# Kernel tuning notes

Measured on AMD Instinct MI355X. Metric: run time of the kernel, lower is better.

Reference implementation:

```python
import jax, jax.numpy as jnp
import numpy as np

DIM = 3072
HEADS = 24
HEAD_DIM = 128
INNER = HEADS * HEAD_DIM
EPS = 1e-6
B, IMG_LEN, TXT_LEN = 1, 2048, 512
S = IMG_LEN + TXT_LEN


def setup_inputs() -> dict:
    key = jax.random.key(0)
    ks = jax.random.split(key, 16)
    w = lambda k, shp: (jax.random.normal(k, shp, dtype=jnp.float32) * 0.02)
    return {
        "x": jax.random.normal(ks[0], (B, IMG_LEN, DIM), dtype=jnp.float32),
        "ctx": jax.random.normal(ks[1], (B, TXT_LEN, DIM), dtype=jnp.float32),
        "rope_cos": jax.random.uniform(ks[2], (S, HEAD_DIM), dtype=jnp.float32),
        "rope_sin": jax.random.uniform(ks[3], (S, HEAD_DIM), dtype=jnp.float32),
        "wq": w(ks[4], (INNER, DIM)),
        "wk": w(ks[5], (INNER, DIM)),
        "wv": w(ks[6], (INNER, DIM)),
        "gq": jnp.ones((HEAD_DIM,), jnp.float32),
        "gk": jnp.ones((HEAD_DIM,), jnp.float32),
        "wo": w(ks[7], (DIM, INNER)),
        "awq": w(ks[8], (INNER, DIM)),
        "awk": w(ks[9], (INNER, DIM)),
        "awv": w(ks[10], (INNER, DIM)),
        "agq": jnp.ones((HEAD_DIM,), jnp.float32),
        "agk": jnp.ones((HEAD_DIM,), jnp.float32),
        "awo": w(ks[11], (DIM, INNER)),
    }


def _rms_norm(t, g):
    # t: [b, s, h, d]; normalize over last dim
    var = jnp.mean(t * t, axis=-1, keepdims=True)
    return t * jax.lax.rsqrt(var + EPS) * g


def _heads(t):
    # [b, s, h*d] -> [b, s, h, d]
    b, s, _ = t.shape
    return t.reshape(b, s, HEADS, HEAD_DIM)


def _apply_rope(t, cos, sin):
    # t: [b, s, h, d]; cos/sin: [s, d] interleaved-pair layout (diffusers Flux style)
    b, s, h, d = t.shape
    x = t.reshape(b, s, h, d // 2, 2)
    rot = jnp.stack([-x[..., 1], x[..., 0]], axis=-1).reshape(b, s, h, d)
    c = cos[None, :, None, :]
    si = sin[None, :, None, :]
    return t * c + rot * si


def reference(x, ctx, rope_cos, rope_sin, wq, wk, wv, gq, gk, wo,
              awq, awk, awv, agq, agk, awo):
    # image-stream QKV + per-head RMSNorm on q,k
    q = _rms_norm(_heads(x @ wq.T), gq)
    k = _rms_norm(_heads(x @ wk.T), gk)
    v = _heads(x @ wv.T)
    # context-stream QKV
    qc = _rms_norm(_heads(ctx @ awq.T), agq)
    kc = _rms_norm(_heads(ctx @ awk.T), agk)
    vc = _heads(ctx @ awv.T)
    # joint streams: [ctx, img] ordering (out[:, :txt_len] is context)
    q = jnp.concatenate([qc, q], axis=1)
    k = jnp.concatenate([kc, k], axis=1)
    v = jnp.concatenate([vc, v], axis=1)
    q = _apply_rope(q, rope_cos, rope_sin)
    k = _apply_rope(k, rope_cos, rope_sin)
    # SDPA
    scale = 1.0 / jnp.sqrt(jnp.float32(HEAD_DIM))
    scores = jnp.einsum('bqhd,bkhd->bhqk', q, k) * scale
    probs = jax.nn.softmax(scores, axis=-1)
    out = jnp.einsum('bhqk,bkhd->bqhd', probs, v)
    out = out.reshape(out.shape[0], out.shape[1], INNER)
    img_out = out[:, TXT_LEN:] @ wo.T
    txt_out = out[:, :TXT_LEN] @ awo.T
    return (img_out, txt_out)
```

## Files before the change

### kernel.cpp

```cpp
#include <hip/hip_runtime.h>
#include <hip/hip_bf16.h>

#define DIMC 3072
#define NHEADS 24
#define HD 128
#define SEQ 2560
#define TXTLEN 512
#define IMGLEN 2048

using short8 = __attribute__((ext_vector_type(8))) short;
using f32x4  = __attribute__((ext_vector_type(4))) float;

static __device__ __forceinline__ float bf2f(unsigned short u) {
    unsigned v = ((unsigned)u) << 16;
    return __builtin_bit_cast(float, v);
}
static __device__ __forceinline__ unsigned short f2bf(float f) {
    unsigned u = __builtin_bit_cast(unsigned, f);
    return (unsigned short)((u + 0x7FFFu + ((u >> 16) & 1u)) >> 16);
}
static __device__ __forceinline__ void gload16(const void* g, void* l) {
    __builtin_amdgcn_global_load_lds((const __attribute__((address_space(1))) unsigned int*)g,
                                     (__attribute__((address_space(3))) unsigned int*)l,
                                     16, 0, 0);
}

__global__ __launch_bounds__(256)
void castk(const float* __restrict__ in, unsigned short* __restrict__ out, int n8)
{
    const int i = blockIdx.x * 256 + threadIdx.x;
    if (i >= n8) return;
    const float4 a = *reinterpret_cast<const float4*>(in + (size_t)i * 8);
    const float4 b = *reinterpret_cast<const float4*>(in + (size_t)i * 8 + 4);
    short8 o;
    o[0] = (short)f2bf(a.x); o[1] = (short)f2bf(a.y);
    o[2] = (short)f2bf(a.z); o[3] = (short)f2bf(a.w);
    o[4] = (short)f2bf(b.x); o[5] = (short)f2bf(b.y);
    o[6] = (short)f2bf(b.z); o[7] = (short)f2bf(b.w);
    *reinterpret_cast<short8*>(out + (size_t)i * 8) = o;
}

struct QkvArgs {
    const unsigned short* A;
    const unsigned short* w0[3];
    const unsigned short* w1[3];
    unsigned short* c[3];
};

__global__ __launch_bounds__(256)
void gemm_qkv(QkvArgs args)
{
    __shared__ unsigned short As[128 * 32];
    __shared__ unsigned short Bs[128 * 32];

    const int bm = blockIdx.x;
    int bn = blockIdx.y;
    const int which = bn / 24; bn -= which * 24;
    const int rowbase = bm * 128, colbase = bn * 128;
    const unsigned short* __restrict__ A = args.A;
    const unsigned short* __restrict__ W = (rowbase < TXTLEN) ? args.w0[which] : args.w1[which];
    unsigned short* __restrict__ C = args.c[which];

    const int t = threadIdx.x, w = t >> 6, l = t & 63;
    const int lr = l & 15, lk = l >> 4;
    const int wr = (w >> 1) * 64, wc = (w & 1) * 64;

    f32x4 acc[4][4] = {};

    const unsigned short* Ag = A + (size_t)(rowbase + w * 32 + (l >> 2)) * DIMC + (l & 3) * 8;
    const unsigned short* Wg = W + (size_t)(colbase + w * 32 + (l >> 2)) * DIMC + (l & 3) * 8;
    unsigned short* AsB = &As[w * 1024];
    unsigned short* BsB = &Bs[w * 1024];

    for (int k0 = 0; k0 < DIMC; k0 += 32) {
        gload16(Ag + k0,            AsB);
        gload16(Ag + 16 * DIMC + k0, AsB + 512);
        gload16(Wg + k0,            BsB);
        gload16(Wg + 16 * DIMC + k0, BsB + 512);
        __syncthreads();
        short8 af[4], bf[4];
#pragma unroll
        for (int m = 0; m < 4; ++m)
            af[m] = *reinterpret_cast<const short8*>(&As[(wr + m * 16 + lr) * 32 + lk * 8]);
#pragma unroll
        for (int n = 0; n < 4; ++n)
            bf[n] = *reinterpret_cast<const short8*>(&Bs[(wc + n * 16 + lr) * 32 + lk * 8]);
#pragma unroll
        for (int m = 0; m < 4; ++m)
#pragma unroll
            for (int n = 0; n < 4; ++n)
                acc[m][n] = __builtin_amdgcn_mfma_f32_16x16x32_bf16(af[m], bf[n], acc[m][n], 0, 0, 0);
        __syncthreads();
    }

#pragma unroll
    for (int m = 0; m < 4; ++m) {
#pragma unroll
        for (int r = 0; r < 4; ++r) {
            const int row = rowbase + wr + m * 16 + lk * 4 + r;
            unsigned short* crow = C + (size_t)row * DIMC + colbase + wc;
#pragma unroll
            for (int n = 0; n < 4; ++n)
                crow[n * 16 + lr] = f2bf(acc[m][n][r]);
        }
    }
}

__global__ __launch_bounds__(256)
void gemm_out(const unsigned short* __restrict__ A, const unsigned short* __restrict__ W0,
              const unsigned short* __restrict__ W1, float* __restrict__ Ctxt,
              float* __restrict__ Cimg)
{
    __shared__ unsigned short As[128 * 32];
    __shared__ unsigned short Bs[128 * 32];

    const int bm = blockIdx.x, bn = blockIdx.y;
    const int rowbase = bm * 128, colbase = bn * 128;
    const unsigned short* __restrict__ W = (rowbase < TXTLEN) ? W0 : W1;

    const int t = threadIdx.x, w = t >> 6, l = t & 63;
    const int lr = l & 15, lk = l >> 4;
    const int wr = (w >> 1) * 64, wc = (w & 1) * 64;

    f32x4 acc[4][4] = {};

    const unsigned short* Ag = A + (size_t)(rowbase + w * 32 + (l >> 2)) * DIMC + (l & 3) * 8;
    const unsigned short* Wg = W + (size_t)(colbase + w * 32 + (l >> 2)) * DIMC + (l & 3) * 8;
    unsigned short* AsB = &As[w * 1024];
    unsigned short* BsB = &Bs[w * 1024];

    for (int k0 = 0; k0 < DIMC; k0 += 32) {
        gload16(Ag + k0,            AsB);
        gload16(Ag + 16 * DIMC + k0, AsB + 512);
        gload16(Wg + k0,            BsB);
        gload16(Wg + 16 * DIMC + k0, BsB + 512);
        __syncthreads();
        short8 af[4], bf[4];
#pragma unroll
        for (int m = 0; m < 4; ++m)
            af[m] = *reinterpret_cast<const short8*>(&As[(wr + m * 16 + lr) * 32 + lk * 8]);
#pragma unroll
        for (int n = 0; n < 4; ++n)
            bf[n] = *reinterpret_cast<const short8*>(&Bs[(wc + n * 16 + lr) * 32 + lk * 8]);
#pragma unroll
        for (int m = 0; m < 4; ++m)
#pragma unroll
            for (int n = 0; n < 4; ++n)
                acc[m][n] = __builtin_amdgcn_mfma_f32_16x16x32_bf16(af[m], bf[n], acc[m][n], 0, 0, 0);
        __syncthreads();
    }

    float* Cb; int rloc;
    if (rowbase < TXTLEN) { Cb = Ctxt; rloc = rowbase; }
    else                  { Cb = Cimg; rloc = rowbase - TXTLEN; }
#pragma unroll
    for (int m = 0; m < 4; ++m) {
#pragma unroll
        for (int r = 0; r < 4; ++r) {
            const int row = rloc + wr + m * 16 + lk * 4 + r;
            float* crow = Cb + (size_t)row * DIMC + colbase + wc;
#pragma unroll
            for (int n = 0; n < 4; ++n)
                crow[n * 16 + lr] = acc[m][n][r];
        }
    }
}

__global__ __launch_bounds__(256)
void normrope(unsigned short* __restrict__ Q, unsigned short* __restrict__ K,
              const float* __restrict__ gq, const float* __restrict__ gk,
              const float* __restrict__ agq, const float* __restrict__ agk,
              const float* __restrict__ rc, const float* __restrict__ rs)
{
    const int wid  = (blockIdx.x << 2) + (threadIdx.x >> 6);
    const int lane = threadIdx.x & 63;
    const int s = wid / NHEADS, h = wid - s * NHEADS;
    const bool img = (s >= TXTLEN);
    const float* gq_ = img ? gq : agq;
    const float* gk_ = img ? gk : agk;

    const size_t base = (size_t)s * DIMC + h * HD + lane * 2;
    const float2 c2  = *reinterpret_cast<const float2*>(rc + (size_t)s * HD + lane * 2);
    const float2 s2  = *reinterpret_cast<const float2*>(rs + (size_t)s * HD + lane * 2);
    const float2 gqv = *reinterpret_cast<const float2*>(gq_ + lane * 2);
    const float2 gkv = *reinterpret_cast<const float2*>(gk_ + lane * 2);

    {
        unsigned pr = *reinterpret_cast<unsigned*>(Q + base);
        float vx = bf2f((unsigned short)(pr & 0xffff));
        float vy = bf2f((unsigned short)(pr >> 16));
        float ss = vx * vx + vy * vy;
#pragma unroll
        for (int off = 1; off < 64; off <<= 1) ss += __shfl_xor(ss, off);
        const float rr = rsqrtf(ss * (1.f / HD) + 1e-6f);
        const float txv = vx * rr * gqv.x, tyv = vy * rr * gqv.y;
        const float qs = 0.08838834764831845f;
        const float ox = (txv * c2.x - tyv * s2.x) * qs;
        const float oy = (tyv * c2.y + txv * s2.y) * qs;
        *reinterpret_cast<unsigned*>(Q + base) = (unsigned)f2bf(ox) | ((unsigned)f2bf(oy) << 16);
    }
    {
        unsigned pr = *reinterpret_cast<unsigned*>(K + base);
        float vx = bf2f((unsigned short)(pr & 0xffff));
        float vy = bf2f((unsigned short)(pr >> 16));
        float ss = vx * vx + vy * vy;
#pragma unroll
        for (int off = 1; off < 64; off <<= 1) ss += __shfl_xor(ss, off);
        const float rr = rsqrtf(ss * (1.f / HD) + 1e-6f);
        const float txv = vx * rr * gkv.x, tyv = vy * rr * gkv.y;
        const float ox = txv * c2.x - tyv * s2.x;
        const float oy = tyv * c2.y + txv * s2.y;
        *reinterpret_cast<unsigned*>(K + base) = (unsigned)f2bf(ox) | ((unsigned)f2bf(oy) << 16);
    }
}

__global__ __launch_bounds__(256)
void transpose_v(const unsigned short* __restrict__ V, unsigned short* __restrict__ Vt)
{
    __shared__ unsigned short Ts[64][136];
    const int kt = blockIdx.x, h = blockIdx.y;
    const int t = threadIdx.x;
#pragma unroll
    for (int p = 0; p < 4; ++p) {
        const int row = p * 16 + (t >> 4);
        const int col = (t & 15) * 8;
        *reinterpret_cast<short8*>(&Ts[row][col]) =
            *reinterpret_cast<const short8*>(V + (size_t)(kt * 64 + row) * DIMC + h * HD + col);
    }
    __syncthreads();
    const int d = t >> 1, kh = t & 1;
    unsigned short* dst = Vt + (size_t)h * HD * SEQ + (size_t)d * SEQ + kt * 64 + kh * 32;
#pragma unroll
    for (int j4 = 0; j4 < 4; ++j4) {
        short8 o;
#pragma unroll
        for (int j = 0; j < 8; ++j) o[j] = (short)Ts[kh * 32 + j4 * 8 + j][d];
        *reinterpret_cast<short8*>(dst + j4 * 8) = o;
    }
}

__global__ __launch_bounds__(256)
void attn_mfma(const unsigned short* __restrict__ Q, const unsigned short* __restrict__ K,
               const unsigned short* __restrict__ Vt, unsigned short* __restrict__ O)
{
    __shared__ unsigned short Ks[64 * 128];
    __shared__ unsigned short Vs[128 * 64];
    __shared__ unsigned short Ps[4][16 * 64];

    const int bq = blockIdx.x, h = blockIdx.y;
    const int t = threadIdx.x, w = t >> 6, l = t & 63;
    const int lr = l & 15, lk = l >> 4;
    const int q0 = bq * 64 + w * 16;

    short8 qf[4];
#pragma unroll
    for (int kk = 0; kk < 4; ++kk)
        qf[kk] = *reinterpret_cast<const short8*>(
            Q + (size_t)(q0 + lr) * DIMC + h * HD + kk * 32 + lk * 8);

    f32x4 oacc[8] = {};
    float mrow[4] = {-1e30f, -1e30f, -1e30f, -1e30f};
    float lrow[4] = {};

    const unsigned short* Kg[4];
    const unsigned short* Vg[4];
#pragma unroll
    for (int c = 0; c < 4; ++c) {
        const int krow = w * 16 + c * 4 + lk;
        const int dsl  = lr ^ (krow & 7);
        Kg[c] = K + (size_t)krow * DIMC + h * HD + dsl * 8;
        const int vd   = w * 32 + c * 8 + (l >> 3);
        const int kvsl = (l & 7) ^ (vd & 7);
        Vg[c] = Vt + (size_t)h * HD * SEQ + (size_t)vd * SEQ + kvsl * 8;
    }

    for (int kt = 0; kt < SEQ / 64; ++kt) {
        const int kv0 = kt * 64;
        __syncthreads();
#pragma unroll
        for (int c = 0; c < 4; ++c) {
            gload16(Kg[c] + (size_t)kv0 * DIMC, &Ks[(w * 4 + c) * 512]);
            gload16(Vg[c] + kv0,                &Vs[(w * 4 + c) * 512]);
        }
        __syncthreads();

        f32x4 sf[4] = {};
#pragma unroll
        for (int nf = 0; nf < 4; ++nf) {
            const int row = nf * 16 + lr;
            const int sw = (row & 7) << 3;
#pragma unroll
            for (int kk = 0; kk < 4; ++kk) {
                short8 bfr = *reinterpret_cast<const short8*>(
                    &Ks[row * 128 + ((kk * 32 + lk * 8) ^ sw)]);
                sf[nf] = __builtin_amdgcn_mfma_f32_16x16x32_bf16(qf[kk], bfr, sf[nf], 0, 0, 0);
            }
        }

        float alpha[4];
#pragma unroll
        for (int r = 0; r < 4; ++r) {
            float mx = fmaxf(fmaxf(sf[0][r], sf[1][r]), fmaxf(sf[2][r], sf[3][r]));
#pragma unroll
            for (int off = 1; off < 16; off <<= 1) mx = fmaxf(mx, __shfl_xor(mx, off));
            const float mn = fmaxf(mrow[r], mx);
            alpha[r] = __expf(mrow[r] - mn);
            mrow[r] = mn;
            float ps = 0.f;
#pragma unroll
            for (int nf = 0; nf < 4; ++nf) {
                const float p = __expf(sf[nf][r] - mn);
                sf[nf][r] = p;
                ps += p;
            }
#pragma unroll
            for (int off = 1; off < 16; off <<= 1) ps += __shfl_xor(ps, off);
            lrow[r] = lrow[r] * alpha[r] + ps;
        }
#pragma unroll
        for (int nf = 0; nf < 8; ++nf)
#pragma unroll
            for (int r = 0; r < 4; ++r) oacc[nf][r] *= alpha[r];

#pragma unroll
        for (int r = 0; r < 4; ++r) {
            const int prow = lk * 4 + r;
            const int sw = (prow & 7) << 3;
#pragma unroll
            for (int nf = 0; nf < 4; ++nf) {
                const int col = nf * 16 + lr;
                Ps[w][prow * 64 + (col ^ sw)] = f2bf(sf[nf][r]);
            }
        }

#pragma unroll
        for (int ks = 0; ks < 2; ++ks) {
            short8 pa = *reinterpret_cast<const short8*>(
                &Ps[w][lr * 64 + ((ks * 32 + lk * 8) ^ ((lr & 7) << 3))]);
#pragma unroll
            for (int nf = 0; nf < 8; ++nf) {
                const int vrow = nf * 16 + lr;
                short8 vf = *reinterpret_cast<const short8*>(
                    &Vs[vrow * 64 + ((ks * 32 + lk * 8) ^ ((vrow & 7) << 3))]);
                oacc[nf] = __builtin_amdgcn_mfma_f32_16x16x32_bf16(pa, vf, oacc[nf], 0, 0, 0);
            }
        }
    }

    float inv[4];
#pragma unroll
    for (int r = 0; r < 4; ++r) inv[r] = 1.f / lrow[r];
#pragma unroll
    for (int nf = 0; nf < 8; ++nf)
#pragma unroll
        for (int r = 0; r < 4; ++r)
            O[(size_t)(q0 + lk * 4 + r) * DIMC + h * HD + nf * 16 + lr] = f2bf(oacc[nf][r] * inv[r]);
}

extern "C" void kernel_launch(void* const* d_in, const int* in_sizes, int n_in,
                              void* d_out, int out_size, void* d_ws, size_t ws_size,
                              hipStream_t stream)
{
    const float* x    = (const float*)d_in[0];
    const float* ctx  = (const float*)d_in[1];
    const float* rc   = (const float*)d_in[2];
    const float* rs   = (const float*)d_in[3];
    const float* wq   = (const float*)d_in[4];
    const float* wk   = (const float*)d_in[5];
    const float* wv   = (const float*)d_in[6];
    const float* gq   = (const float*)d_in[7];
    const float* gk   = (const float*)d_in[8];
    const float* wo   = (const float*)d_in[9];
    const float* awq  = (const float*)d_in[10];
    const float* awk  = (const float*)d_in[11];
    const float* awv  = (const float*)d_in[12];
    const float* agq  = (const float*)d_in[13];
    const float* agk  = (const float*)d_in[14];
    const float* awo  = (const float*)d_in[15];

    unsigned short* wsp = (unsigned short*)d_ws;
    const size_t SZ  = (size_t)SEQ * DIMC;
    const size_t WSZ = (size_t)DIMC * DIMC;
    unsigned short* XC  = wsp;
    unsigned short* Qb  = XC + SZ;
    unsigned short* Kb  = Qb + SZ;
    unsigned short* Vb  = Kb + SZ;
    unsigned short* Vtb = Vb + SZ;
    unsigned short* Ob  = Vtb + SZ;
    unsigned short* Wc[8];
    for (int i = 0; i < 8; ++i) Wc[i] = Ob + SZ + (size_t)i * WSZ;

    auto cast = [&](const float* src, unsigned short* dst, size_t n) {
        const int n8 = (int)(n / 8);
        castk<<<dim3((n8 + 255) / 256), dim3(256), 0, stream>>>(src, dst, n8);
    };
    cast(ctx, XC, (size_t)TXTLEN * DIMC);
    cast(x,   XC + (size_t)TXTLEN * DIMC, (size_t)IMGLEN * DIMC);
    cast(awq, Wc[0], WSZ); cast(wq, Wc[1], WSZ);
    cast(awk, Wc[2], WSZ); cast(wk, Wc[3], WSZ);
    cast(awv, Wc[4], WSZ); cast(wv, Wc[5], WSZ);
    cast(awo, Wc[6], WSZ); cast(wo, Wc[7], WSZ);

    QkvArgs qa;
    qa.A = XC;
    qa.w0[0] = Wc[0]; qa.w1[0] = Wc[1]; qa.c[0] = Qb;
    qa.w0[1] = Wc[2]; qa.w1[1] = Wc[3]; qa.c[1] = Kb;
    qa.w0[2] = Wc[4]; qa.w1[2] = Wc[5]; qa.c[2] = Vb;
    gemm_qkv<<<dim3(SEQ / 128, 72), dim3(256), 0, stream>>>(qa);

    normrope<<<dim3(SEQ * NHEADS / 4), dim3(256), 0, stream>>>(Qb, Kb, gq, gk, agq, agk, rc, rs);

    transpose_v<<<dim3(SEQ / 64, NHEADS), dim3(256), 0, stream>>>(Vb, Vtb);

    attn_mfma<<<dim3(SEQ / 64, NHEADS), dim3(256), 0, stream>>>(Qb, Kb, Vtb, Ob);

    float* out = (float*)d_out;
    gemm_out<<<dim3(SEQ / 128, DIMC / 128), dim3(256), 0, stream>>>(
        Ob, Wc[6], Wc[7], out + (size_t)IMGLEN * DIMC, out);
}
```

Measured before the change: 601.8 us.

## Fuse RMSNorm+RoPE into QKV GEMM epilogue, double-buffer attention, batch weight casts

```diff
diff --git a/kernel.cpp b/kernel.cpp
--- a/kernel.cpp
+++ b/kernel.cpp
@@ -40,11 +40,30 @@
     *reinterpret_cast<short8*>(out + (size_t)i * 8) = o;
 }
 
+struct W8 { const float* src[8]; };
+__global__ __launch_bounds__(256)
+void castw(W8 a, unsigned short* __restrict__ dstbase, int n8, size_t wsz)
+{
+    const int i = blockIdx.x * 256 + threadIdx.x;
+    if (i >= n8) return;
+    const float* in = a.src[blockIdx.y];
+    unsigned short* out = dstbase + (size_t)blockIdx.y * wsz;
+    const float4 av = *reinterpret_cast<const float4*>(in + (size_t)i * 8);
+    const float4 bv = *reinterpret_cast<const float4*>(in + (size_t)i * 8 + 4);
+    short8 o;
+    o[0] = (short)f2bf(av.x); o[1] = (short)f2bf(av.y);
+    o[2] = (short)f2bf(av.z); o[3] = (short)f2bf(av.w);
+    o[4] = (short)f2bf(bv.x); o[5] = (short)f2bf(bv.y);
+    o[6] = (short)f2bf(bv.z); o[7] = (short)f2bf(bv.w);
+    *reinterpret_cast<short8*>(out + (size_t)i * 8) = o;
+}
+
 struct QkvArgs {
     const unsigned short* A;
     const unsigned short* w0[3];
     const unsigned short* w1[3];
     unsigned short* c[3];
+    const float *gq, *gk, *agq, *agk, *rc, *rs;
 };
 
 __global__ __launch_bounds__(256)
@@ -63,9 +82,8 @@
 
     const int t = threadIdx.x, w = t >> 6, l = t & 63;
     const int lr = l & 15, lk = l >> 4;
-    const int wr = (w >> 1) * 64, wc = (w & 1) * 64;
-
-    f32x4 acc[4][4] = {};
+
+    f32x4 acc[2][8] = {};
 
     const unsigned short* Ag = A + (size_t)(rowbase + w * 32 + (l >> 2)) * DIMC + (l & 3) * 8;
     const unsigned short* Wg = W + (size_t)(colbase + w * 32 + (l >> 2)) * DIMC + (l & 3) * 8;
@@ -73,35 +91,69 @@
     unsigned short* BsB = &Bs[w * 1024];
 
     for (int k0 = 0; k0 < DIMC; k0 += 32) {
-        gload16(Ag + k0,            AsB);
+        gload16(Ag + k0,             AsB);
         gload16(Ag + 16 * DIMC + k0, AsB + 512);
-        gload16(Wg + k0,            BsB);
+        gload16(Wg + k0,             BsB);
         gload16(Wg + 16 * DIMC + k0, BsB + 512);
         __syncthreads();
-        short8 af[4], bf[4];
-#pragma unroll
-        for (int m = 0; m < 4; ++m)
-            af[m] = *reinterpret_cast<const short8*>(&As[(wr + m * 16 + lr) * 32 + lk * 8]);
-#pragma unroll
-        for (int n = 0; n < 4; ++n)
-            bf[n] = *reinterpret_cast<const short8*>(&Bs[(wc + n * 16 + lr) * 32 + lk * 8]);
-#pragma unroll
-        for (int m = 0; m < 4; ++m)
-#pragma unroll
-            for (int n = 0; n < 4; ++n)
+        short8 af[2], bf[8];
+#pragma unroll
+        for (int m = 0; m < 2; ++m)
+            af[m] = *reinterpret_cast<const short8*>(&As[(w * 32 + m * 16 + lr) * 32 + lk * 8]);
+#pragma unroll
+        for (int n = 0; n < 8; ++n)
+            bf[n] = *reinterpret_cast<const short8*>(&Bs[(n * 16 + lr) * 32 + lk * 8]);
+#pragma unroll
+        for (int m = 0; m < 2; ++m)
+#pragma unroll
+            for (int n = 0; n < 8; ++n)
                 acc[m][n] = __builtin_amdgcn_mfma_f32_16x16x32_bf16(af[m], bf[n], acc[m][n], 0, 0, 0);
         __syncthreads();
     }
 
-#pragma unroll
-    for (int m = 0; m < 4; ++m) {
-#pragma unroll
-        for (int r = 0; r < 4; ++r) {
-            const int row = rowbase + wr + m * 16 + lk * 4 + r;
-            unsigned short* crow = C + (size_t)row * DIMC + colbase + wc;
-#pragma unroll
-            for (int n = 0; n < 4; ++n)
-                crow[n * 16 + lr] = f2bf(acc[m][n][r]);
+    if (which < 2) {
+        const float* gg = (which == 0) ? ((rowbase < TXTLEN) ? args.agq : args.gq)
+                                       : ((rowbase < TXTLEN) ? args.agk : args.gk);
+        const float qscale = (which == 0) ? 0.08838834764831845f : 1.0f;
+        float gcol[8];
+#pragma unroll
+        for (int n = 0; n < 8; ++n) gcol[n] = gg[n * 16 + lr];
+
+#pragma unroll
+        for (int m = 0; m < 2; ++m) {
+#pragma unroll
+            for (int r = 0; r < 4; ++r) {
+                const int srow = rowbase + w * 32 + m * 16 + lk * 4 + r;
+                float ss = 0.f;
+#pragma unroll
+                for (int n = 0; n < 8; ++n) ss += acc[m][n][r] * acc[m][n][r];
+#pragma unroll
+                for (int off = 1; off < 16; off <<= 1) ss += __shfl_xor(ss, off);
+                const float rn = rsqrtf(ss * (1.f / HD) + 1e-6f);
+                unsigned short* crow = C + (size_t)srow * DIMC + colbase;
+                const float* crs = args.rc + (size_t)srow * HD;
+                const float* srs = args.rs + (size_t)srow * HD;
+#pragma unroll
+                for (int n = 0; n < 8; ++n) {
+                    const int col = n * 16 + lr;
+                    const float v = acc[m][n][r] * rn * gcol[n];
+                    const float pv = __shfl_xor(v, 1);
+                    const float o = (v * crs[col] + ((lr & 1) ? pv : -pv) * srs[col]) * qscale;
+                    crow[col] = f2bf(o);
+                }
+            }
+        }
+    } else {
+#pragma unroll
+        for (int m = 0; m < 2; ++m) {
+#pragma unroll
+            for (int r = 0; r < 4; ++r) {
+                const int srow = rowbase + w * 32 + m * 16 + lk * 4 + r;
+                unsigned short* crow = C + (size_t)srow * DIMC + colbase;
+#pragma unroll
+                for (int n = 0; n < 8; ++n)
+                    crow[n * 16 + lr] = f2bf(acc[m][n][r]);
+            }
         }
     }
 }
@@ -130,9 +182,9 @@
     unsigned short* BsB = &Bs[w * 1024];
 
     for (int k0 = 0; k0 < DIMC; k0 += 32) {
-        gload16(Ag + k0,            AsB);
+        gload16(Ag + k0,             AsB);
         gload16(Ag + 16 * DIMC + k0, AsB + 512);
-        gload16(Wg + k0,            BsB);
+        gload16(Wg + k0,             BsB);
         gload16(Wg + 16 * DIMC + k0, BsB + 512);
         __syncthreads();
         short8 af[4], bf[4];
@@ -163,54 +215,6 @@
             for (int n = 0; n < 4; ++n)
                 crow[n * 16 + lr] = acc[m][n][r];
         }
-    }
-}
-
-__global__ __launch_bounds__(256)
-void normrope(unsigned short* __restrict__ Q, unsigned short* __restrict__ K,
-              const float* __restrict__ gq, const float* __restrict__ gk,
-              const float* __restrict__ agq, const float* __restrict__ agk,
-              const float* __restrict__ rc, const float* __restrict__ rs)
-{
-    const int wid  = (blockIdx.x << 2) + (threadIdx.x >> 6);
-    const int lane = threadIdx.x & 63;
-    const int s = wid / NHEADS, h = wid - s * NHEADS;
-    const bool img = (s >= TXTLEN);
-    const float* gq_ = img ? gq : agq;
-    const float* gk_ = img ? gk : agk;
-
-    const size_t base = (size_t)s * DIMC + h * HD + lane * 2;
-    const float2 c2  = *reinterpret_cast<const float2*>(rc + (size_t)s * HD + lane * 2);
-    const float2 s2  = *reinterpret_cast<const float2*>(rs + (size_t)s * HD + lane * 2);
-    const float2 gqv = *reinterpret_cast<const float2*>(gq_ + lane * 2);
-    const float2 gkv = *reinterpret_cast<const float2*>(gk_ + lane * 2);
-
-    {
-        unsigned pr = *reinterpret_cast<unsigned*>(Q + base);
-        float vx = bf2f((unsigned short)(pr & 0xffff));
-        float vy = bf2f((unsigned short)(pr >> 16));
-        float ss = vx * vx + vy * vy;
-#pragma unroll
-        for (int off = 1; off < 64; off <<= 1) ss += __shfl_xor(ss, off);
-        const float rr = rsqrtf(ss * (1.f / HD) + 1e-6f);
-        const float txv = vx * rr * gqv.x, tyv = vy * rr * gqv.y;
-        const float qs = 0.08838834764831845f;
-        const float ox = (txv * c2.x - tyv * s2.x) * qs;
-        const float oy = (tyv * c2.y + txv * s2.y) * qs;
-        *reinterpret_cast<unsigned*>(Q + base) = (unsigned)f2bf(ox) | ((unsigned)f2bf(oy) << 16);
-    }
-    {
-        unsigned pr = *reinterpret_cast<unsigned*>(K + base);
-        float vx = bf2f((unsigned short)(pr & 0xffff));
-        float vy = bf2f((unsigned short)(pr >> 16));
-        float ss = vx * vx + vy * vy;
-#pragma unroll
-        for (int off = 1; off < 64; off <<= 1) ss += __shfl_xor(ss, off);
-        const float rr = rsqrtf(ss * (1.f / HD) + 1e-6f);
-        const float txv = vx * rr * gkv.x, tyv = vy * rr * gkv.y;
-        const float ox = txv * c2.x - tyv * s2.x;
-        const float oy = tyv * c2.y + txv * s2.y;
-        *reinterpret_cast<unsigned*>(K + base) = (unsigned)f2bf(ox) | ((unsigned)f2bf(oy) << 16);
     }
 }
 
@@ -239,18 +243,18 @@
     }
 }
 
-__global__ __launch_bounds__(256)
+__global__ __launch_bounds__(512)
 void attn_mfma(const unsigned short* __restrict__ Q, const unsigned short* __restrict__ K,
                const unsigned short* __restrict__ Vt, unsigned short* __restrict__ O)
 {
-    __shared__ unsigned short Ks[64 * 128];
-    __shared__ unsigned short Vs[128 * 64];
-    __shared__ unsigned short Ps[4][16 * 64];
+    __shared__ unsigned short Ks[2][64 * 128];
+    __shared__ unsigned short Vs[2][128 * 64];
+    __shared__ unsigned short Ps[8][16 * 64];
 
     const int bq = blockIdx.x, h = blockIdx.y;
     const int t = threadIdx.x, w = t >> 6, l = t & 63;
     const int lr = l & 15, lk = l >> 4;
-    const int q0 = bq * 64 + w * 16;
+    const int q0 = bq * 128 + w * 16;
 
     short8 qf[4];
 #pragma unroll
@@ -262,27 +266,34 @@
     float mrow[4] = {-1e30f, -1e30f, -1e30f, -1e30f};
     float lrow[4] = {};
 
-    const unsigned short* Kg[4];
-    const unsigned short* Vg[4];
-#pragma unroll
-    for (int c = 0; c < 4; ++c) {
-        const int krow = w * 16 + c * 4 + lk;
-        const int dsl  = lr ^ (krow & 7);
-        Kg[c] = K + (size_t)krow * DIMC + h * HD + dsl * 8;
-        const int vd   = w * 32 + c * 8 + (l >> 3);
-        const int kvsl = (l & 7) ^ (vd & 7);
-        Vg[c] = Vt + (size_t)h * HD * SEQ + (size_t)vd * SEQ + kvsl * 8;
-    }
-
-    for (int kt = 0; kt < SEQ / 64; ++kt) {
-        const int kv0 = kt * 64;
+    const unsigned short* Kg[2];
+    const unsigned short* Vg[2];
+    int krow_[2], vrow_[2];
+#pragma unroll
+    for (int i = 0; i < 2; ++i) {
+        const int kr = w * 8 + i * 4 + (l >> 4);
+        krow_[i] = kr;
+        Kg[i] = K + (size_t)kr * DIMC + h * HD + (((l & 15) ^ (kr & 7)) * 8);
+        const int vr = w * 16 + i * 8 + (l >> 3);
+        vrow_[i] = vr;
+        Vg[i] = Vt + (size_t)h * HD * SEQ + (size_t)vr * SEQ + (((l & 7) ^ (vr & 7)) * 8);
+    }
+
+    auto STAGE = [&](int buf, int kv0) {
+#pragma unroll
+        for (int i = 0; i < 2; ++i) {
+            gload16(Kg[i] + (size_t)kv0 * DIMC, &Ks[buf][(w * 8 + i * 4) * 128]);
+            gload16(Vg[i] + kv0,                &Vs[buf][(w * 16 + i * 8) * 64]);
+        }
+    };
+
+    STAGE(0, 0);
+
+    constexpr int NT = SEQ / 64;
+    for (int kt = 0; kt < NT; ++kt) {
+        const int buf = kt & 1;
         __syncthreads();
-#pragma unroll
-        for (int c = 0; c < 4; ++c) {
-            gload16(Kg[c] + (size_t)kv0 * DIMC, &Ks[(w * 4 + c) * 512]);
-            gload16(Vg[c] + kv0,                &Vs[(w * 4 + c) * 512]);
-        }
-        __syncthreads();
+        if (kt + 1 < NT) STAGE(buf ^ 1, (kt + 1) * 64);
 
         f32x4 sf[4] = {};
 #pragma unroll
@@ -292,7 +303,7 @@
 #pragma unroll
             for (int kk = 0; kk < 4; ++kk) {
                 short8 bfr = *reinterpret_cast<const short8*>(
-                    &Ks[row * 128 + ((kk * 32 + lk * 8) ^ sw)]);
+                    &Ks[buf][row * 128 + ((kk * 32 + lk * 8) ^ sw)]);
                 sf[nf] = __builtin_amdgcn_mfma_f32_16x16x32_bf16(qf[kk], bfr, sf[nf], 0, 0, 0);
             }
         }
@@ -341,7 +352,7 @@
             for (int nf = 0; nf < 8; ++nf) {
                 const int vrow = nf * 16 + lr;
                 short8 vf = *reinterpret_cast<const short8*>(
-                    &Vs[vrow * 64 + ((ks * 32 + lk * 8) ^ ((vrow & 7) << 3))]);
+                    &Vs[buf][vrow * 64 + ((ks * 32 + lk * 8) ^ ((vrow & 7) << 3))]);
                 oacc[nf] = __builtin_amdgcn_mfma_f32_16x16x32_bf16(pa, vf, oacc[nf], 0, 0, 0);
             }
         }
@@ -387,34 +398,35 @@
     unsigned short* Vb  = Kb + SZ;
     unsigned short* Vtb = Vb + SZ;
     unsigned short* Ob  = Vtb + SZ;
-    unsigned short* Wc[8];
-    for (int i = 0; i < 8; ++i) Wc[i] = Ob + SZ + (size_t)i * WSZ;
-
-    auto cast = [&](const float* src, unsigned short* dst, size_t n) {
-        const int n8 = (int)(n / 8);
-        castk<<<dim3((n8 + 255) / 256), dim3(256), 0, stream>>>(src, dst, n8);
-    };
-    cast(ctx, XC, (size_t)TXTLEN * DIMC);
-    cast(x,   XC + (size_t)TXTLEN * DIMC, (size_t)IMGLEN * DIMC);
-    cast(awq, Wc[0], WSZ); cast(wq, Wc[1], WSZ);
-    cast(awk, Wc[2], WSZ); cast(wk, Wc[3], WSZ);
-    cast(awv, Wc[4], WSZ); cast(wv, Wc[5], WSZ);
-    cast(awo, Wc[6], WSZ); cast(wo, Wc[7], WSZ);
+    unsigned short* Wc  = Ob + SZ;
+
+    {
+        int n8 = (int)((size_t)TXTLEN * DIMC / 8);
+        castk<<<dim3((n8 + 255) / 256), dim3(256), 0, stream>>>(ctx, XC, n8);
+        n8 = (int)((size_t)IMGLEN * DIMC / 8);
+        castk<<<dim3((n8 + 255) / 256), dim3(256), 0, stream>>>(x, XC + (size_t)TXTLEN * DIMC, n8);
+    }
+    {
+        W8 w8;
+        w8.src[0] = awq; w8.src[1] = wq; w8.src[2] = awk; w8.src[3] = wk;
+        w8.src[4] = awv; w8.src[5] = wv; w8.src[6] = awo; w8.src[7] = wo;
+        const int n8 = (int)(WSZ / 8);
+        castw<<<dim3((n8 + 255) / 256, 8), dim3(256), 0, stream>>>(w8, Wc, n8, WSZ);
+    }
 
     QkvArgs qa;
     qa.A = XC;
-    qa.w0[0] = Wc[0]; qa.w1[0] = Wc[1]; qa.c[0] = Qb;
-    qa.w0[1] = Wc[2]; qa.w1[1] = Wc[3]; qa.c[1] = Kb;
-    qa.w0[2] = Wc[4]; qa.w1[2] = Wc[5]; qa.c[2] = Vb;
+    qa.w0[0] = Wc + 0 * WSZ; qa.w1[0] = Wc + 1 * WSZ; qa.c[0] = Qb;
+    qa.w0[1] = Wc + 2 * WSZ; qa.w1[1] = Wc + 3 * WSZ; qa.c[1] = Kb;
+    qa.w0[2] = Wc + 4 * WSZ; qa.w1[2] = Wc + 5 * WSZ; qa.c[2] = Vb;
+    qa.gq = gq; qa.gk = gk; qa.agq = agq; qa.agk = agk; qa.rc = rc; qa.rs = rs;
     gemm_qkv<<<dim3(SEQ / 128, 72), dim3(256), 0, stream>>>(qa);
 
-    normrope<<<dim3(SEQ * NHEADS / 4), dim3(256), 0, stream>>>(Qb, Kb, gq, gk, agq, agk, rc, rs);
-
     transpose_v<<<dim3(SEQ / 64, NHEADS), dim3(256), 0, stream>>>(Vb, Vtb);
 
-    attn_mfma<<<dim3(SEQ / 64, NHEADS), dim3(256), 0, stream>>>(Qb, Kb, Vtb, Ob);
+    attn_mfma<<<dim3(SEQ / 128, NHEADS), dim3(512), 0, stream>>>(Qb, Kb, Vtb, Ob);
 
     float* out = (float*)d_out;
     gemm_out<<<dim3(SEQ / 128, DIMC / 128), dim3(256), 0, stream>>>(
-        Ob, Wc[6], Wc[7], out + (size_t)IMGLEN * DIMC, out);
-}
+        Ob, Wc + 6 * WSZ, Wc + 7 * WSZ, out + (size_t)IMGLEN * DIMC, out);
+}
```

New measurement: 642.9 us. 6.8% more time.
